# Performance work log

Hardware: AMD Instinct MI355X
Metric: run time of the kernel (lower is better)

The kernel has to match this reference:

```python
import jax, jax.numpy as jnp
import numpy as np

N_NODES = 100000
N_EDGES = 3200000


def setup_inputs() -> dict:
    key = jax.random.key(0)
    ks = jax.random.split(key, 20)
    x = jax.random.normal(ks[0], (N_NODES, 3), dtype=jnp.float32)
    edge_index = jax.random.randint(ks[1], (2, N_EDGES), 0, N_NODES, dtype=jnp.int64)

    def w(k, shape, fan_in):
        return jax.random.normal(k, shape, dtype=jnp.float32) * (1.0 / np.sqrt(fan_in))

    return {
        "x": x, "edge_index": edge_index,
        # layer 1: in=3, out=16, heads=2
        "W1": w(ks[2], (3, 32), 3), "a_src1": w(ks[3], (2, 16), 16), "a_dst1": w(ks[4], (2, 16), 16), "b1": jnp.zeros((32,), jnp.float32),
        # layer 2: in=32, out=16, heads=2
        "W2": w(ks[5], (32, 32), 32), "a_src2": w(ks[6], (2, 16), 16), "a_dst2": w(ks[7], (2, 16), 16), "b2": jnp.zeros((32,), jnp.float32),
        # layer 3: in=32, out=16, heads=1
        "W3": w(ks[8], (32, 16), 32), "a_src3": w(ks[9], (1, 16), 16), "a_dst3": w(ks[10], (1, 16), 16), "b3": jnp.zeros((16,), jnp.float32),
        # output linear 16 -> 1
        "Wout": w(ks[11], (16, 1), 16), "bout": jnp.zeros((1,), jnp.float32),
    }


def gat_layer(x, src, dst, W, a_src, a_dst, b, heads, ch, n):
    # h: [N, H, C]
    h = (x @ W).reshape(n, heads, ch)
    alpha_src = jnp.sum(h * a_src[None], axis=-1)  # [N, H]
    alpha_dst = jnp.sum(h * a_dst[None], axis=-1)  # [N, H]
    e = jax.nn.leaky_relu(alpha_src[src] + alpha_dst[dst], 0.2)  # [E, H]
    # segment softmax over incoming edges of each dst node
    m = jax.ops.segment_max(e, dst, num_segments=n)
    m = jnp.where(jnp.isfinite(m), m, 0.0)
    ex = jnp.exp(e - jax.lax.stop_gradient(m)[dst])
    s = jax.ops.segment_sum(ex, dst, num_segments=n)
    alpha = ex / (s[dst] + 1e-16)  # [E, H]
    out = jax.ops.segment_sum(h[src] * alpha[:, :, None], dst, num_segments=n)  # [N, H, C]
    return out.reshape(n, heads * ch) + b


def reference(x, edge_index, W1, a_src1, a_dst1, b1, W2, a_src2, a_dst2, b2,
              W3, a_src3, a_dst3, b3, Wout, bout):
    n = x.shape[0]
    loops = jnp.arange(n, dtype=edge_index.dtype)
    src = jnp.concatenate([edge_index[0], loops])  # PyG add_self_loops=True
    dst = jnp.concatenate([edge_index[1], loops])
    h = jax.nn.elu(gat_layer(x, src, dst, W1, a_src1, a_dst1, b1, 2, 16, n))
    h = jax.nn.elu(gat_layer(h, src, dst, W2, a_src2, a_dst2, b2, 2, 16, n))
    h = jax.nn.elu(gat_layer(h, src, dst, W3, a_src3, a_dst3, b3, 1, 16, n))
    embeddings = h
    out = jax.nn.sigmoid(h @ Wout + bout)
    return out, embeddings
```

## Files before the change

kernel.cpp:

```cpp
#include <hip/hip_runtime.h>
#include <hip/hip_fp16.h>
#include <math.h>

#define TPB 256
#define PMAX 128
#define PSH 10
#define PW  1024
#define CHUNK 2048
#define KPT 8
#define PCAP 38912
#define PCSTR 16

__device__ __forceinline__ float leaky02(float x) { return x > 0.f ? x : 0.2f * x; }
__device__ __forceinline__ float eluf(float x) { return x > 0.f ? x : (__expf(x) - 1.f); }


__global__ __launch_bounds__(256) void scatter_kernel(const int* __restrict__ src,
                                                      const int* __restrict__ dst,
                                                      int E, int n,
                                                      int* __restrict__ pcursor,
                                                      unsigned* __restrict__ pstage) {
  __shared__ int lcnt[4][PMAX];
  __shared__ int ltot[PMAX];
  __shared__ int lscan[PMAX];
  __shared__ int lbase[PMAX];
  __shared__ int wtot;
  __shared__ unsigned slab[CHUNK];
  int t = threadIdx.x;
  int wid = t >> 6;
  int lane = t & 63;
  int Etot = E + n;
  int c0 = blockIdx.x * CHUNK;
  if (c0 >= Etot) return;
  int c1 = min(c0 + CHUNK, Etot);
  for (int j = t; j < 4 * PMAX; j += TPB) ((int*)lcnt)[j] = 0;

  int dd[KPT], ss[KPT];
  bool vv[KPT];
#pragma unroll
  for (int k = 0; k < KPT; ++k) {
    int idx = c0 + t + k * TPB;
    vv[k] = idx < c1;
    if (vv[k]) {
      if (idx < E) { ss[k] = src[idx]; dd[k] = dst[idx]; }
      else         { ss[k] = dd[k] = idx - E; }
    } else { ss[k] = 0; dd[k] = 0; }
  }
  __syncthreads();
#pragma unroll
  for (int k = 0; k < KPT; ++k)
    if (vv[k]) atomicAdd(&lcnt[wid][dd[k] >> PSH], 1);
  __syncthreads();
  int tot = 0, x = 0;
  if (t < PMAX) {
    int a0 = lcnt[0][t], a1 = lcnt[1][t], a2 = lcnt[2][t], a3 = lcnt[3][t];
    tot = a0 + a1 + a2 + a3;
    ltot[t] = tot;
    lcnt[0][t] = 0; lcnt[1][t] = a0; lcnt[2][t] = a0 + a1; lcnt[3][t] = a0 + a1 + a2;
    x = tot;
#pragma unroll
    for (int off = 1; off < 64; off <<= 1) {
      int u = __shfl_up(x, off);
      if (lane >= off) x += u;
    }
    if (t == 63) wtot = x;
  }
  __syncthreads();
  if (t < PMAX) {
    lscan[t] = x - tot + ((t >= 64) ? wtot : 0);
    lbase[t] = tot ? atomicAdd(&pcursor[t * PCSTR], tot) : 0;
  }
  __syncthreads();
#pragma unroll
  for (int k = 0; k < KPT; ++k) {
    if (vv[k]) {
      int p = dd[k] >> PSH;
      int sub = atomicAdd(&lcnt[wid][p], 1);
      slab[lscan[p] + sub] = ((unsigned)ss[k] << PSH) | (unsigned)(dd[k] & (PW - 1));
    }
  }
  __syncthreads();
  for (int p = wid; p < PMAX; p += 4) {
    int cnt = ltot[p];
    int s = lscan[p];
    size_t b = (size_t)p * PCAP + lbase[p];
    for (int j = lane; j < cnt; j += 64)
      pstage[b + j] = slab[s + j];
  }
}

__global__ __launch_bounds__(1024) void build_csr_kernel(const unsigned* __restrict__ pstage,
                                                         const int* __restrict__ pcursor,
                                                         int nvtx,
                                                         int* __restrict__ rowptr,
                                                         int* __restrict__ csr_src) {
  __shared__ int ssum[PMAX];
  __shared__ int lhist[PW];
  __shared__ int lcur[PW];
  int t = threadIdx.x;
  int lane = t & 63;
  int wid = t >> 6;
  int p = blockIdx.x;
  size_t rbase = (size_t)p * PCAP;
  if (t < PMAX) ssum[t] = pcursor[t * PCSTR];
  lhist[t] = 0;
  __syncthreads();
  for (int off = 1; off < PMAX; off <<= 1) {
    int a = 0;
    if (t < PMAX && t >= off) a = ssum[t - off];
    __syncthreads();
    if (t < PMAX) ssum[t] += a;
    __syncthreads();
  }
  int cnt = pcursor[p * PCSTR];
  int wbase = ssum[p] - cnt;
  int nodebase = p << PSH;
  for (int i = t; i < cnt; i += 4096) {
    unsigned w[4]; bool vv[4];
#pragma unroll
    for (int k = 0; k < 4; ++k) {
      int j = i + k * 1024;
      vv[k] = j < cnt;
      w[k] = vv[k] ? pstage[rbase + j] : 0u;
    }
#pragma unroll
    for (int k = 0; k < 4; ++k)
      if (vv[k]) atomicAdd(&lhist[w[k] & (PW - 1)], 1);
  }
  __syncthreads();
  int v = lhist[t];
  int x = v;
#pragma unroll
  for (int off = 1; off < 64; off <<= 1) {
    int u = __shfl_up(x, off);
    if (lane >= off) x += u;
  }
  if (lane == 63) lcur[wid] = x;
  __syncthreads();
  if (t < 16) {
    int wsum = lcur[t];
    int y = wsum;
#pragma unroll
    for (int off = 1; off < 16; off <<= 1) {
      int u = __shfl_up(y, off);
      if (t >= off) y += u;
    }
    lcur[t] = y - wsum;
  }
  __syncthreads();
  int acc = wbase + x + lcur[wid] - v;
  __syncthreads();
  lcur[t] = acc;
  int node = nodebase + t;
  if (node < nvtx) rowptr[node] = acc;
  __syncthreads();
  for (int i = t; i < cnt; i += 4096) {
    unsigned w[4]; bool vv[4];
#pragma unroll
    for (int k = 0; k < 4; ++k) {
      int j = i + k * 1024;
      vv[k] = j < cnt;
      w[k] = vv[k] ? pstage[rbase + j] : 0u;
    }
#pragma unroll
    for (int k = 0; k < 4; ++k) {
      if (vv[k]) {
        int pos = atomicAdd(&lcur[w[k] & (PW - 1)], 1);
        csr_src[pos] = (int)(w[k] >> PSH);
      }
    }
  }
  if (p == (int)gridDim.x - 1 && t == 0) rowptr[nvtx] = wbase + cnt;
}


template<int IN, int OUT, int H>
__global__ void transform_kernel(const float* __restrict__ x, const float* __restrict__ W,
                                 const float* __restrict__ a_src, const float* __restrict__ a_dst,
                                 __half* __restrict__ h, float* __restrict__ asrc,
                                 float* __restrict__ adst, int n) {
  __shared__ float sW[IN * OUT];
  __shared__ float sa[2 * OUT];
  for (int i = threadIdx.x; i < IN * OUT; i += blockDim.x) sW[i] = W[i];
  if (threadIdx.x < OUT) {
    sa[threadIdx.x] = a_src[threadIdx.x];
    sa[OUT + threadIdx.x] = a_dst[threadIdx.x];
  }
  __syncthreads();
  int i = blockIdx.x * blockDim.x + threadIdx.x;
  if (i >= n) return;
  float xv[IN];
#pragma unroll
  for (int k = 0; k < IN; k++) xv[k] = x[(size_t)i * IN + k];
  float hv[OUT];
#pragma unroll
  for (int j = 0; j < OUT; j++) {
    float acc = 0.f;
#pragma unroll
    for (int k = 0; k < IN; k++) acc += xv[k] * sW[k * OUT + j];
    hv[j] = acc;
  }
#pragma unroll
  for (int j = 0; j < OUT; j += 2)
    ((__half2*)h)[((size_t)i * OUT + j) >> 1] = __floats2half2_rn(hv[j], hv[j + 1]);
#pragma unroll
  for (int hh = 0; hh < H; hh++) {
    float as = 0.f, ad = 0.f;
#pragma unroll
    for (int c = 0; c < 16; c++) {
      as += hv[hh * 16 + c] * sa[hh * 16 + c];
      ad += hv[hh * 16 + c] * sa[OUT + hh * 16 + c];
    }
    asrc[i * H + hh] = as;
    adst[i * H + hh] = ad;
  }
}


template<int NIT>
__device__ __forceinline__ void gat12_gather(const float2* __restrict__ sp,
                                             const uint2* __restrict__ hfp,
                                             int q, int g, float4& acc) {
  float2 p[NIT];
#pragma unroll
  for (int it = 0; it < NIT; ++it) p[it] = sp[2 * (g + it * 8)];
  uint2 hv[NIT];
#pragma unroll
  for (int it = 0; it < NIT; ++it) hv[it] = hfp[__float_as_int(p[it].x) + q];
#pragma unroll
  for (int it = 0; it < NIT; ++it) {
    float2 fa = __half22float2(*(const __half2*)&hv[it].x);
    float2 fb = __half22float2(*(const __half2*)&hv[it].y);
    float w = p[it].y;
    acc.x += w * fa.x; acc.y += w * fa.y;
    acc.z += w * fb.x; acc.w += w * fb.y;
  }
}

__device__ __forceinline__ void gat12_gather_t(const float2* sp, const uint2* hfp,
                                               int q, int g, int cnt, float4& acc) {
  if (cnt <= 32)      gat12_gather<4>(sp, hfp, q, g, acc);
  else if (cnt <= 48) gat12_gather<6>(sp, hfp, q, g, acc);
  else                gat12_gather<8>(sp, hfp, q, g, acc);
}

__global__ __launch_bounds__(256) void node_gat12(
    const int* __restrict__ rowptr,
    const int* __restrict__ csr_src,
    const float* __restrict__ asrc,
    const float* __restrict__ adst,
    const __half* __restrict__ hfeat,
    const float* __restrict__ bias,
    float* __restrict__ outb,
    int n) {
  __shared__ float4 s_e[4][64];
  int wid = threadIdx.x >> 6;
  int lane = threadIdx.x & 63;
  int i = (blockIdx.x * blockDim.x + threadIdx.x) >> 6;
  if (i >= n) return;
  int start = rowptr[i];
  int d = rowptr[i + 1] - start;
  float ad0 = adst[i * 2 + 0];
  float ad1 = adst[i * 2 + 1];
  const uint2* hfp = (const uint2*)hfeat;
  const float2* asrc2 = (const float2*)asrc;
  int g = lane >> 3;
  int q = lane & 7;
  const float2* sp = (const float2*)(&s_e[wid][0]) + (q >> 2);
  float4 acc = make_float4(0.f, 0.f, 0.f, 0.f);
  float sl0 = 0.f, sl1 = 0.f;

  if (d <= 64) {
    int sidx8 = 0;
    float w0 = 0.f, w1 = 0.f;
    if (lane < d) {
      int sidx = csr_src[start + lane];
      sidx8 = sidx << 3;
      float2 av = asrc2[sidx];
      w0 = __expf(leaky02(av.x + ad0));
      w1 = __expf(leaky02(av.y + ad1));
    }
    sl0 = w0; sl1 = w1;
    s_e[wid][lane] = make_float4(__int_as_float(sidx8), w0, __int_as_float(sidx8), w1);
    gat12_gather_t(sp, hfp, q, g, d, acc);
  } else {
    for (int base = 0; base < d; base += 64) {
      int k = base + lane;
      int sidx8 = 0;
      float w0 = 0.f, w1 = 0.f;
      if (k < d) {
        int sidx = csr_src[start + k];
        sidx8 = sidx << 3;
        float2 av = asrc2[sidx];
        w0 = __expf(leaky02(av.x + ad0));
        w1 = __expf(leaky02(av.y + ad1));
        sl0 += w0; sl1 += w1;
      }
      s_e[wid][lane] = make_float4(__int_as_float(sidx8), w0, __int_as_float(sidx8), w1);
      int cnt = min(64, d - base);
      gat12_gather_t(sp, hfp, q, g, cnt, acc);
    }
  }

#pragma unroll
  for (int off = 32; off >= 1; off >>= 1) {
    sl0 += __shfl_xor(sl0, off);
    sl1 += __shfl_xor(sl1, off);
  }
#pragma unroll
  for (int off = 8; off <= 32; off <<= 1) {
    acc.x += __shfl_xor(acc.x, off);
    acc.y += __shfl_xor(acc.y, off);
    acc.z += __shfl_xor(acc.z, off);
    acc.w += __shfl_xor(acc.w, off);
  }
  if (lane < 8) {
    float inv = 1.f / (((lane >= 4) ? sl1 : sl0) + 1e-16f);
    float4 bv = ((const float4*)bias)[lane];
    float4 o;
    o.x = eluf(acc.x * inv + bv.x);
    o.y = eluf(acc.y * inv + bv.y);
    o.z = eluf(acc.z * inv + bv.z);
    o.w = eluf(acc.w * inv + bv.w);
    ((float4*)outb)[(size_t)i * 8 + lane] = o;
  }
}

template<int NIT>
__device__ __forceinline__ void gat3_gather(const float2* __restrict__ sp,
                                            const unsigned* __restrict__ hfp,
                                            int q, int g, float2& acc) {
  float2 p[NIT];
#pragma unroll
  for (int it = 0; it < NIT; ++it) p[it] = sp[g + it * 8];
  unsigned hv[NIT];
#pragma unroll
  for (int it = 0; it < NIT; ++it) hv[it] = hfp[__float_as_int(p[it].x) + q];
#pragma unroll
  for (int it = 0; it < NIT; ++it) {
    float2 f = __half22float2(*(const __half2*)&hv[it]);
    float w = p[it].y;
    acc.x += w * f.x; acc.y += w * f.y;
  }
}

__device__ __forceinline__ void gat3_gather_t(const float2* sp, const unsigned* hfp,
                                              int q, int g, int cnt, float2& acc) {
  if (cnt <= 32)      gat3_gather<4>(sp, hfp, q, g, acc);
  else if (cnt <= 48) gat3_gather<6>(sp, hfp, q, g, acc);
  else                gat3_gather<8>(sp, hfp, q, g, acc);
}

__global__ __launch_bounds__(256) void node_gat3(
    const int* __restrict__ rowptr,
    const int* __restrict__ csr_src,
    const float* __restrict__ asrc,
    const float* __restrict__ adst,
    const __half* __restrict__ hfeat,
    const float* __restrict__ b3,
    const float* __restrict__ Wout,
    const float* __restrict__ bout,
    float* __restrict__ out,
    int n) {
  __shared__ float2 s_hw[4][64];
  int wid = threadIdx.x >> 6;
  int lane = threadIdx.x & 63;
  int i = (blockIdx.x * blockDim.x + threadIdx.x) >> 6;
  if (i >= n) return;
  int start = rowptr[i];
  int d = rowptr[i + 1] - start;
  float ad0 = adst[i];
  const unsigned* hfp = (const unsigned*)hfeat;
  int g = lane >> 3;
  int q = lane & 7;
  const float2* sp = s_hw[wid];
  float2 acc = make_float2(0.f, 0.f);
  float sl = 0.f;

  if (d <= 64) {
    int sidx8 = 0;
    float w0 = 0.f;
    if (lane < d) {
      int sidx = csr_src[start + lane];
      sidx8 = sidx << 3;
      w0 = __expf(leaky02(asrc[sidx] + ad0));
    }
    sl = w0;
    s_hw[wid][lane] = make_float2(__int_as_float(sidx8), w0);
    gat3_gather_t(sp, hfp, q, g, d, acc);
  } else {
    for (int base = 0; base < d; base += 64) {
      int k = base + lane;
      int sidx8 = 0;
      float w0 = 0.f;
      if (k < d) {
        int sidx = csr_src[start + k];
        sidx8 = sidx << 3;
        w0 = __expf(leaky02(asrc[sidx] + ad0));
        sl += w0;
      }
      s_hw[wid][lane] = make_float2(__int_as_float(sidx8), w0);
      int cnt = min(64, d - base);
      gat3_gather_t(sp, hfp, q, g, cnt, acc);
    }
  }

#pragma unroll
  for (int off = 32; off >= 1; off >>= 1) sl += __shfl_xor(sl, off);
#pragma unroll
  for (int off = 8; off <= 32; off <<= 1) {
    acc.x += __shfl_xor(acc.x, off);
    acc.y += __shfl_xor(acc.y, off);
  }
  float z = 0.f;
  if (lane < 8) {
    float inv = 1.f / (sl + 1e-16f);
    float2 bv = ((const float2*)b3)[lane];
    float2 wv = ((const float2*)Wout)[lane];
    float2 o;
    o.x = eluf(acc.x * inv + bv.x);
    o.y = eluf(acc.y * inv + bv.y);
    ((float2*)(out + n))[(size_t)i * 8 + lane] = o;
    z = o.x * wv.x + o.y * wv.y;
  }
  z += __shfl_xor(z, 1);
  z += __shfl_xor(z, 2);
  z += __shfl_xor(z, 4);
  if (lane == 0) out[i] = 1.f / (1.f + __expf(-(z + bout[0])));
}


extern "C" void kernel_launch(void* const* d_in, const int* in_sizes, int n_in,
                              void* d_out, int out_size, void* d_ws, size_t ws_size,
                              hipStream_t stream) {
  const float* x    = (const float*)d_in[0];
  const int*   ei   = (const int*)d_in[1];
  const float* W1   = (const float*)d_in[2];
  const float* as1  = (const float*)d_in[3];
  const float* ad1  = (const float*)d_in[4];
  const float* b1   = (const float*)d_in[5];
  const float* W2   = (const float*)d_in[6];
  const float* as2  = (const float*)d_in[7];
  const float* ad2  = (const float*)d_in[8];
  const float* b2   = (const float*)d_in[9];
  const float* W3   = (const float*)d_in[10];
  const float* as3  = (const float*)d_in[11];
  const float* ad3  = (const float*)d_in[12];
  const float* b3   = (const float*)d_in[13];
  const float* Wout = (const float*)d_in[14];
  const float* bout = (const float*)d_in[15];
  float* out = (float*)d_out;

  const int n = in_sizes[0] / 3;
  const int E = in_sizes[1] / 2;
  const int Etot = E + n;
  const int* src = ei;
  const int* dst = ei + E;
  const int nbC = (Etot + CHUNK - 1) / CHUNK;
  const int NP = ((n - 1) >> PSH) + 1;

  float* ws = (float*)d_ws;
  float* bufH = ws;
  float* bufX = bufH + (size_t)n * 32;
  float* asrc = bufX + (size_t)n * 32;
  float* adst = asrc + (size_t)n * 2;
  int* rowptr  = (int*)(adst + (size_t)n * 2);
  int* pcursor = rowptr + n + 1;
  int* csr_src = pcursor + PMAX * PCSTR;
  unsigned* pstage = (unsigned*)ws;
  __half* hH = (__half*)bufH;

  const int nbN = (n + TPB - 1) / TPB;
  const int nbW = (n + 3) / 4;

  hipMemsetAsync(pcursor, 0, PMAX * PCSTR * sizeof(int), stream);
  scatter_kernel<<<nbC, TPB, 0, stream>>>(src, dst, E, n, pcursor, pstage);
  build_csr_kernel<<<NP, 1024, 0, stream>>>(pstage, pcursor, n, rowptr, csr_src);

  transform_kernel<3, 32, 2><<<nbN, TPB, 0, stream>>>(x, W1, as1, ad1, hH, asrc, adst, n);
  node_gat12<<<nbW, TPB, 0, stream>>>(rowptr, csr_src, asrc, adst, hH, b1, bufX, n);

  transform_kernel<32, 32, 2><<<nbN, TPB, 0, stream>>>(bufX, W2, as2, ad2, hH, asrc, adst, n);
  node_gat12<<<nbW, TPB, 0, stream>>>(rowptr, csr_src, asrc, adst, hH, b2, bufX, n);

  transform_kernel<32, 16, 1><<<nbN, TPB, 0, stream>>>(bufX, W3, as3, ad3, hH, asrc, adst, n);
  node_gat3<<<nbW, TPB, 0, stream>>>(rowptr, csr_src, asrc, adst, hH, b3, Wout, bout, out, n);
}
```

Baseline: 351.1 us.

## Write scatter output directly to global and specialize gather unroll per count

The scatter kernel drops its shared-memory slab, the prefix scan and the coalesced copy-out. Each edge is now written straight to its partition's global staging slot, which cuts LDS traffic and two barriers but gives scattered, uncoalesced global writes. Separately, the gather helpers dispatch to eight template instantiations based on ceil(cnt/8) instead of three, so padded iterations are avoided for low-degree nodes. The extra instantiations add code size and branch divergence.

```diff
diff --git a/kernel.cpp b/kernel.cpp
--- a/kernel.cpp
+++ b/kernel.cpp
@@ -21,14 +21,9 @@
                                                       int* __restrict__ pcursor,
                                                       unsigned* __restrict__ pstage) {
   __shared__ int lcnt[4][PMAX];
-  __shared__ int ltot[PMAX];
-  __shared__ int lscan[PMAX];
   __shared__ int lbase[PMAX];
-  __shared__ int wtot;
-  __shared__ unsigned slab[CHUNK];
   int t = threadIdx.x;
   int wid = t >> 6;
-  int lane = t & 63;
   int Etot = E + n;
   int c0 = blockIdx.x * CHUNK;
   if (c0 >= Etot) return;
@@ -51,23 +46,10 @@
   for (int k = 0; k < KPT; ++k)
     if (vv[k]) atomicAdd(&lcnt[wid][dd[k] >> PSH], 1);
   __syncthreads();
-  int tot = 0, x = 0;
   if (t < PMAX) {
     int a0 = lcnt[0][t], a1 = lcnt[1][t], a2 = lcnt[2][t], a3 = lcnt[3][t];
-    tot = a0 + a1 + a2 + a3;
-    ltot[t] = tot;
+    int tot = a0 + a1 + a2 + a3;
     lcnt[0][t] = 0; lcnt[1][t] = a0; lcnt[2][t] = a0 + a1; lcnt[3][t] = a0 + a1 + a2;
-    x = tot;
-#pragma unroll
-    for (int off = 1; off < 64; off <<= 1) {
-      int u = __shfl_up(x, off);
-      if (lane >= off) x += u;
-    }
-    if (t == 63) wtot = x;
-  }
-  __syncthreads();
-  if (t < PMAX) {
-    lscan[t] = x - tot + ((t >= 64) ? wtot : 0);
     lbase[t] = tot ? atomicAdd(&pcursor[t * PCSTR], tot) : 0;
   }
   __syncthreads();
@@ -76,16 +58,9 @@
     if (vv[k]) {
       int p = dd[k] >> PSH;
       int sub = atomicAdd(&lcnt[wid][p], 1);
-      slab[lscan[p] + sub] = ((unsigned)ss[k] << PSH) | (unsigned)(dd[k] & (PW - 1));
-    }
-  }
-  __syncthreads();
-  for (int p = wid; p < PMAX; p += 4) {
-    int cnt = ltot[p];
-    int s = lscan[p];
-    size_t b = (size_t)p * PCAP + lbase[p];
-    for (int j = lane; j < cnt; j += 64)
-      pstage[b + j] = slab[s + j];
+      pstage[(size_t)p * PCAP + lbase[p] + sub] =
+          ((unsigned)ss[k] << PSH) | (unsigned)(dd[k] & (PW - 1));
+    }
   }
 }
 
@@ -239,9 +214,16 @@
 
 __device__ __forceinline__ void gat12_gather_t(const float2* sp, const uint2* hfp,
                                                int q, int g, int cnt, float4& acc) {
-  if (cnt <= 32)      gat12_gather<4>(sp, hfp, q, g, acc);
-  else if (cnt <= 48) gat12_gather<6>(sp, hfp, q, g, acc);
-  else                gat12_gather<8>(sp, hfp, q, g, acc);
+  switch ((cnt + 7) >> 3) {
+    case 1: gat12_gather<1>(sp, hfp, q, g, acc); break;
+    case 2: gat12_gather<2>(sp, hfp, q, g, acc); break;
+    case 3: gat12_gather<3>(sp, hfp, q, g, acc); break;
+    case 4: gat12_gather<4>(sp, hfp, q, g, acc); break;
+    case 5: gat12_gather<5>(sp, hfp, q, g, acc); break;
+    case 6: gat12_gather<6>(sp, hfp, q, g, acc); break;
+    case 7: gat12_gather<7>(sp, hfp, q, g, acc); break;
+    default: gat12_gather<8>(sp, hfp, q, g, acc); break;
+  }
 }
 
 __global__ __launch_bounds__(256) void node_gat12(
@@ -346,9 +328,16 @@
 
 __device__ __forceinline__ void gat3_gather_t(const float2* sp, const unsigned* hfp,
                                               int q, int g, int cnt, float2& acc) {
-  if (cnt <= 32)      gat3_gather<4>(sp, hfp, q, g, acc);
-  else if (cnt <= 48) gat3_gather<6>(sp, hfp, q, g, acc);
-  else                gat3_gather<8>(sp, hfp, q, g, acc);
+  switch ((cnt + 7) >> 3) {
+    case 1: gat3_gather<1>(sp, hfp, q, g, acc); break;
+    case 2: gat3_gather<2>(sp, hfp, q, g, acc); break;
+    case 3: gat3_gather<3>(sp, hfp, q, g, acc); break;
+    case 4: gat3_gather<4>(sp, hfp, q, g, acc); break;
+    case 5: gat3_gather<5>(sp, hfp, q, g, acc); break;
+    case 6: gat3_gather<6>(sp, hfp, q, g, acc); break;
+    case 7: gat3_gather<7>(sp, hfp, q, g, acc); break;
+    default: gat3_gather<8>(sp, hfp, q, g, acc); break;
+  }
 }
 
 __global__ __launch_bounds__(256) void node_gat3(
```

After: 352.2 us. About the same (+0.3%).
